# Optimization experiments

Measured on AMD Instinct MI355X. Metric: run time of the kernel, lower is better.

The kernel has to match this reference:

```python
import jax, jax.numpy as jnp
import numpy as np

B_GRAPHS, N2, FDIM, HEADS = 128, 32, 256, 4
TOTAL = 262144


def setup_inputs() -> dict:
    key = jax.random.key(0)
    ks = jax.random.split(key, 6)
    # sorted graph ids, guaranteed to cover all B_GRAPHS values
    batch = jnp.sort(jnp.concatenate([
        jax.random.randint(ks[0], (TOTAL - B_GRAPHS,), 0, B_GRAPHS),
        jnp.arange(B_GRAPHS)])).astype(jnp.int32)
    x = jax.random.normal(ks[1], (TOTAL, FDIM), jnp.float32)
    queries = jax.random.normal(ks[2], (1, N2, FDIM), jnp.float32)
    s = 1.0 / np.sqrt(FDIM)
    in_proj_w = jax.random.uniform(ks[3], (3 * FDIM, FDIM), jnp.float32, -s, s)
    in_proj_b = jnp.zeros((3 * FDIM,), jnp.float32)
    out_proj_w = jax.random.uniform(ks[4], (FDIM, FDIM), jnp.float32, -s, s)
    out_proj_b = jnp.zeros((FDIM,), jnp.float32)
    return {"x": x, "batch": batch, "queries": queries,
            "in_proj_w": in_proj_w, "in_proj_b": in_proj_b,
            "out_proj_w": out_proj_w, "out_proj_b": out_proj_b}


def reference(x, batch, queries, in_proj_w, in_proj_b, out_proj_w, out_proj_b):
    F = x.shape[-1]
    H = HEADS
    d = F // H
    B = int(batch.max()) + 1
    counts = jnp.bincount(batch, length=B)                      # [B]
    N_max = int(counts.max())
    offsets = jnp.concatenate([jnp.zeros((1,), counts.dtype), jnp.cumsum(counts)[:-1]])
    pos = jnp.arange(batch.shape[0]) - offsets[batch]           # position within segment
    # ragged -> padded scatter (equivalent of the python loop)
    x_padded = jnp.zeros((B, N_max, F), x.dtype).at[batch, pos].set(x)
    valid = jnp.arange(N_max)[None, :] < counts[:, None]        # [B, N_max], True = real token

    Wq, Wk, Wv = in_proj_w[:F], in_proj_w[F:2 * F], in_proj_w[2 * F:]
    bq, bk, bv = in_proj_b[:F], in_proj_b[F:2 * F], in_proj_b[2 * F:]

    scale = 1.0 / np.sqrt(d)
    q = (queries[0] @ Wq.T + bq).reshape(N2, H, d) * scale      # [N2, H, d] (shared over B)
    k = (x_padded @ Wk.T + bk).reshape(B, N_max, H, d)
    v = (x_padded @ Wv.T + bv).reshape(B, N_max, H, d)

    scores = jnp.einsum('qhd,bkhd->bhqk', q, k)                 # [B, H, N2, N_max]
    scores = jnp.where(valid[:, None, None, :], scores, -jnp.inf)
    attn = jax.nn.softmax(scores, axis=-1)
    out = jnp.einsum('bhqk,bkhd->bqhd', attn, v).reshape(B, N2, F)
    out = out @ out_proj_w.T + out_proj_b
    return out.reshape(B * N2, F)
```

## Files before the change

### kernel.cpp

```cpp
#include <hip/hip_runtime.h>
#include <hip/hip_bf16.h>

typedef __bf16 bf16x8 __attribute__((ext_vector_type(8)));
typedef float  f32x4  __attribute__((ext_vector_type(4)));

#define MFMA16(a,b,c) __builtin_amdgcn_mfma_f32_16x16x32_bf16((a),(b),(c),0,0,0)

__device__ __forceinline__ unsigned short f2bf(float f){
  unsigned int u = __float_as_uint(f);
  u += 0x7fffu + ((u >> 16) & 1u);
  return (unsigned short)(u >> 16);
}

__device__ __forceinline__ unsigned int cvtpk(float lo, float hi){
  unsigned int r;
  asm("v_cvt_pk_bf16_f32 %0, %1, %2" : "=v"(r) : "v"(lo), "v"(hi));
  return r;
}

__device__ __forceinline__ void block_sync(){
  asm volatile("s_waitcnt lgkmcnt(0)" ::: "memory");
  __builtin_amdgcn_s_barrier();
}

constexpr float SCALE_LOG2E = 0.125f * 1.4426950408889634f;

__global__ void k_prep(const float* __restrict__ queries, const float* __restrict__ ipw,
                       const float* __restrict__ ipb, const float* __restrict__ opw,
                       const float* __restrict__ opb, const int* __restrict__ batch,
                       int total, int* __restrict__ starts,
                       unsigned short* __restrict__ AqF,
                       unsigned short* __restrict__ Cmat, float* __restrict__ cvec)
{
  __shared__ __align__(16) float sh[256];
  __shared__ __align__(16) float sh2[256];
  const int t = threadIdx.x, bid = blockIdx.x;

  if (bid < 32){
    const int q = bid;
    sh[t] = queries[q*256 + t];
    __syncthreads();
    const float* wr = ipw + (size_t)t*256;
    float acc = 0.f;
    #pragma unroll 8
    for (int j = 0; j < 256; j += 4){
      float4 wv = *reinterpret_cast<const float4*>(wr + j);
      float4 qv = *reinterpret_cast<const float4*>(&sh[j]);
      acc += wv.x*qv.x + wv.y*qv.y + wv.z*qv.z + wv.w*qv.w;
    }
    sh2[t] = acc + ipb[t];
    __syncthreads();
    #pragma unroll
    for (int h = 0; h < 4; h++){
      const float* wk = ipw + (size_t)(256 + h*64)*256 + t;
      float a2 = 0.f;
      #pragma unroll 8
      for (int d = 0; d < 64; d++) a2 += sh2[h*64 + d] * wk[(size_t)d*256];
      const int dst = ((h*2 + (q>>4))*8 + (t>>5))*512 + (((t>>3)&3)*16 + (q&15))*8 + (t&7);
      AqF[dst] = f2bf(a2 * SCALE_LOG2E);
    }
  } else if (bid < 288){
    const int g = bid - 32;
    sh[t] = opw[(size_t)g*256 + t];
    __syncthreads();
    #pragma unroll
    for (int h = 0; h < 4; h++){
      const float* wv = ipw + (size_t)(512 + h*64)*256 + t;
      float acc = 0.f;
      #pragma unroll 8
      for (int d = 0; d < 64; d++) acc += wv[(size_t)d*256] * sh[h*64 + d];
      Cmat[(size_t)g*1024 + h*256 + t] = f2bf(acc);
    }
    sh2[t] = ipb[512 + t] * sh[t];
    __syncthreads();
    for (int off = 128; off > 0; off >>= 1){
      if (t < off) sh2[t] += sh2[t + off];
      __syncthreads();
    }
    if (t == 0) cvec[g] = sh2[0] + opb[g];
  } else {
    const int sb = bid - 288;
    const int i0 = sb*1024 + t*4;
    if (i0 + 3 < total){
      if (i0 == 0) starts[0] = 0;
      const int4 b4 = *reinterpret_cast<const int4*>(batch + i0);
      if (b4.y != b4.x) starts[b4.y] = i0 + 1;
      if (b4.z != b4.y) starts[b4.z] = i0 + 2;
      if (b4.w != b4.z) starts[b4.w] = i0 + 3;
      if (i0 + 4 < total){
        const int nxt = batch[i0 + 4];
        if (nxt != b4.w) starts[nxt] = i0 + 4;
      } else {
        starts[128] = total;
      }
    }
  }
}


#define LOADC(c_) { \
  const int c0_ = (c_)*32; \
  _Pragma("unroll") \
  for (int n = 0; n < 4; n++){ \
    int nl_ = c0_ + nq*4 + n; nl_ = nl_ < cnt-1 ? nl_ : cnt-1; \
    rA[n] = *reinterpret_cast<const float2*>(xg + (size_t)nl_*256 + fp*2); } }

#define STAGE(xsP, xtP) { \
  _Pragma("unroll") \
  for (int n = 0; n < 4; n++) \
    *reinterpret_cast<unsigned int*>(&(xsP)[(nq*4 + n)*264 + fp*2]) = cvtpk(rA[n].x, rA[n].y); \
  { const int f0_ = fp*2; \
    uint2 w0_; w0_.x = cvtpk(rA[0].x, rA[1].x); w0_.y = cvtpk(rA[2].x, rA[3].x); \
    *reinterpret_cast<uint2*>(reinterpret_cast<char*>(xtP) + ((f0_*80 + nq*8) ^ (((f0_>>2)&7)<<4))) = w0_; \
    const int f1_ = fp*2 + 1; \
    uint2 w1_; w1_.x = cvtpk(rA[0].y, rA[1].y); w1_.y = cvtpk(rA[2].y, rA[3].y); \
    *reinterpret_cast<uint2*>(reinterpret_cast<char*>(xtP) + ((f1_*80 + nq*8) ^ (((f1_>>2)&7)<<4))) = w1_; } }

__global__ __launch_bounds__(1024, 4) void k_attn(
    const float* __restrict__ x, const int* __restrict__ starts,
    const unsigned short* __restrict__ AqF,
    float* __restrict__ partO, float* __restrict__ partL)
{
  __shared__ __align__(16) unsigned short xsub[2][32*264];
  __shared__ __align__(16) unsigned short xT  [3][256*40];
  __shared__ __align__(16) unsigned short Plds[2][128*40];
  __shared__ __align__(16) float lred[2][128];

  const int tid = threadIdx.x;
  const int wave = tid >> 6, lane = tid & 63, lg = lane >> 4, li = lane & 15;
  const int nq = tid >> 7, fp = tid & 127;
  const int bid = blockIdx.x;
  const int g = bid >> 1, s = bid & 1;
  const int s0 = starts[g], s1 = starts[g+1];
  const int cntg = s1 - s0;
  const int half = (cntg + 1) >> 1;
  const int nstart = s0 + s*half;
  int cnt = cntg - s*half; cnt = cnt < 0 ? 0 : (cnt > half ? half : cnt);
  const int chunks = (cnt + 31) >> 5;
  const float* xg = x + (size_t)nstart*256;
  const int pbase = bid*128;

  float2 rA[4];
  if (chunks > 0){
    LOADC(0);
    STAGE(xsub[0], xT[0]);
    if (chunks > 1) LOADC(1);
    block_sync();
  }

  if (wave < 8){
    const int rg2 = wave >> 1, bsel = wave & 1;
    bf16x8 bfragS[2][8];
    #pragma unroll
    for (int rf = 0; rf < 2; rf++)
      #pragma unroll
      for (int kb = 0; kb < 8; kb++)
        bfragS[rf][kb] = *reinterpret_cast<const bf16x8*>(AqF + (size_t)((rg2*2 + rf)*8 + kb)*512 + lane*8);

    float rsum0 = 0.f, rsum1 = 0.f;
    const int row0 = rg2*32 + li, row1 = rg2*32 + 16 + li;
    const int pbyte0 = (row0*80 + bsel*32 + lg*8) ^ (((row0>>2)&7)<<4);
    const int pbyte1 = (row1*80 + bsel*32 + lg*8) ^ (((row1>>2)&7)<<4);

    int cur3 = 0;
    for (int c = 0; c < chunks; ++c){
      const int cur2 = c & 1;
      const int nxt3 = (cur3 == 2) ? 0 : cur3 + 1;

      f32x4 sc0 = f32x4{0.f,0.f,0.f,0.f}, sc1 = f32x4{0.f,0.f,0.f,0.f};
      __builtin_amdgcn_s_setprio(1);
      #pragma unroll
      for (int kb = 0; kb < 8; kb++){
        const bf16x8 af = *reinterpret_cast<const bf16x8*>(&xsub[cur2][(bsel*16 + li)*264 + kb*32 + lg*8]);
        sc0 = MFMA16(af, bfragS[0][kb], sc0);
        sc1 = MFMA16(af, bfragS[1][kb], sc1);
      }
      __builtin_amdgcn_s_setprio(0);

      const int nodebase = c*32 + bsel*16 + lg*4;
      float p0[4], p1[4];
      #pragma unroll
      for (int r = 0; r < 4; r++){
        const bool v = (nodebase + r) < cnt;
        p0[r] = v ? __builtin_exp2f(sc0[r]) : 0.f;
        p1[r] = v ? __builtin_exp2f(sc1[r]) : 0.f;
        rsum0 += p0[r]; rsum1 += p1[r];
      }
      {
        char* pl = reinterpret_cast<char*>(Plds[cur2]);
        uint2 w0; w0.x = cvtpk(p0[0], p0[1]); w0.y = cvtpk(p0[2], p0[3]);
        uint2 w1; w1.x = cvtpk(p1[0], p1[1]); w1.y = cvtpk(p1[2], p1[3]);
        *reinterpret_cast<uint2*>(pl + pbyte0) = w0;
        *reinterpret_cast<uint2*>(pl + pbyte1) = w1;
      }

      if (c + 1 < chunks){
        STAGE(xsub[cur2 ^ 1], xT[nxt3]);
        if (c + 2 < chunks) LOADC(c + 2);
      }
      block_sync();
      cur3 = nxt3;
    }

    rsum0 += __shfl_xor(rsum0, 16); rsum0 += __shfl_xor(rsum0, 32);
    rsum1 += __shfl_xor(rsum1, 16); rsum1 += __shfl_xor(rsum1, 32);
    if (lane < 16){
      lred[bsel][rg2*32 + li]      = rsum0;
      lred[bsel][rg2*32 + 16 + li] = rsum1;
    }
  } else {
    const int pw = wave - 8, fs = pw*32;
    f32x4 oacc[8][2];
    #pragma unroll
    for (int i = 0; i < 8; i++){ oacc[i][0] = f32x4{0.f,0.f,0.f,0.f}; oacc[i][1] = f32x4{0.f,0.f,0.f,0.f}; }
    const int fr0 = fs + li, fr1 = fs + 16 + li;
    const int bvb0 = (fr0*80 + lg*16) ^ (((fr0>>2)&7)<<4);
    const int bvb1 = (fr1*80 + lg*16) ^ (((fr1>>2)&7)<<4);

    int cur3 = 0;
    for (int c = 0; c < chunks; ++c){
      const int cur2 = c & 1;
      const int nxt3 = (cur3 == 2) ? 0 : cur3 + 1;

      if (c + 1 < chunks){
        STAGE(xsub[cur2 ^ 1], xT[nxt3]);
        if (c + 2 < chunks) LOADC(c + 2);
      }
      block_sync();

      const char* xtC = reinterpret_cast<const char*>(xT[cur3]);
      const bf16x8 bv0 = *reinterpret_cast<const bf16x8*>(xtC + bvb0);
      const bf16x8 bv1 = *reinterpret_cast<const bf16x8*>(xtC + bvb1);
      const char* plC = reinterpret_cast<const char*>(Plds[cur2]);
      __builtin_amdgcn_s_setprio(1);
      #pragma unroll
      for (int rt = 0; rt < 8; rt++){
        const int prow = rt*16 + li;
        const bf16x8 pa = *reinterpret_cast<const bf16x8*>(plC + ((prow*80 + lg*16) ^ (((prow>>2)&7)<<4)));
        oacc[rt][0] = MFMA16(pa, bv0, oacc[rt][0]);
        oacc[rt][1] = MFMA16(pa, bv1, oacc[rt][1]);
      }
      __builtin_amdgcn_s_setprio(0);
      cur3 = nxt3;
    }

    #pragma unroll
    for (int rt = 0; rt < 8; rt++){
      #pragma unroll
      for (int r = 0; r < 4; r++){
        const size_t orow = (size_t)(pbase + rt*16 + lg*4 + r)*256;
        partO[orow + fs + li]      = oacc[rt][0][r];
        partO[orow + fs + 16 + li] = oacc[rt][1][r];
      }
    }
  }

  block_sync();
  if (tid < 128) partL[pbase + tid] = lred[0][tid] + lred[1][tid];
}

__global__ __launch_bounds__(512, 1) void k_out(
    const float* __restrict__ partO, const float* __restrict__ partL,
    const unsigned short* __restrict__ Cmat, const float* __restrict__ cvec,
    float* __restrict__ out)
{
  __shared__ __align__(16) unsigned short plds[16*1024];
  __shared__ float sinv[64];
  const int tid = threadIdx.x;
  const int g = blockIdx.x >> 1, qh = blockIdx.x & 1;
  const int p0 = 2*g, p1 = 2*g + 1;
  if (tid < 64){
    const int h = tid >> 4, qr = tid & 15;
    const int row = h*32 + qh*16 + qr;
    const float L = partL[p0*128 + row] + partL[p1*128 + row];
    sinv[tid] = 1.f / L;
  }
  __syncthreads();
  #pragma unroll
  for (int i = 0; i < 8; i++){
    const int idx = tid + i*512;
    const int qr = idx >> 8;
    const int cg = idx & 255;
    const int h = cg >> 6, f4 = (cg & 63)*4;
    const int row = h*32 + qh*16 + qr;
    const float4 o0 = *reinterpret_cast<const float4*>(&partO[(size_t)(p0*128 + row)*256 + f4]);
    const float4 o1 = *reinterpret_cast<const float4*>(&partO[(size_t)(p1*128 + row)*256 + f4]);
    const float sc = sinv[h*16 + qr];
    uint2 w; w.x = cvtpk((o0.x+o1.x)*sc, (o0.y+o1.y)*sc);
             w.y = cvtpk((o0.z+o1.z)*sc, (o0.w+o1.w)*sc);
    const int col4 = cg*4;
    const int bc = (col4*2) ^ ((qr & 7) << 4);
    *reinterpret_cast<uint2*>(reinterpret_cast<char*>(plds) + qr*2048 + bc) = w;
  }
  __syncthreads();
  const int wave = tid >> 6, lane = tid & 63, lg = lane >> 4, li = lane & 15;
  f32x4 acc0 = {0.f,0.f,0.f,0.f}, acc1 = {0.f,0.f,0.f,0.f};
  const float cv0 = cvec[wave*32 + li], cv1 = cvec[wave*32 + 16 + li];
  const unsigned short* cb0 = Cmat + (size_t)(wave*32 + li)*1024;
  const unsigned short* cb1 = Cmat + (size_t)(wave*32 + 16 + li)*1024;
  #pragma unroll 8
  for (int kb = 0; kb < 32; kb++){
    const int bc = ((kb*32 + lg*8)*2) ^ ((li & 7) << 4);
    const bf16x8 aa = *reinterpret_cast<const bf16x8*>(reinterpret_cast<const char*>(plds) + li*2048 + bc);
    const bf16x8 b0 = *reinterpret_cast<const bf16x8*>(cb0 + kb*32 + lg*8);
    const bf16x8 b1 = *reinterpret_cast<const bf16x8*>(cb1 + kb*32 + lg*8);
    acc0 = MFMA16(aa, b0, acc0);
    acc1 = MFMA16(aa, b1, acc1);
  }
  #pragma unroll
  for (int r = 0; r < 4; r++){
    const int q = lg*4 + r;
    const size_t orow = (size_t)(g*32 + qh*16 + q)*256;
    out[orow + wave*32 + li]      = acc0[r] + cv0;
    out[orow + wave*32 + 16 + li] = acc1[r] + cv1;
  }
}


extern "C" void kernel_launch(void* const* d_in, const int* in_sizes, int n_in,
                              void* d_out, int out_size, void* d_ws, size_t ws_size,
                              hipStream_t stream)
{
  const float* x       = (const float*)d_in[0];
  const int*   batch   = (const int*)d_in[1];
  const float* queries = (const float*)d_in[2];
  const float* ipw     = (const float*)d_in[3];
  const float* ipb     = (const float*)d_in[4];
  const float* opw     = (const float*)d_in[5];
  const float* opb     = (const float*)d_in[6];
  float* out = (float*)d_out;
  const int total = in_sizes[1];

  char* w = (char*)d_ws;
  int*            starts = (int*)(w);
  unsigned short* AqF    = (unsigned short*)(w + 36*1024);
  unsigned short* Cmat   = (unsigned short*)(w + 102*1024);
  float*          cvec   = (float*)(w + 616*1024);
  float*          partO  = (float*)(w + (size_t)1024*1024);
  float*          partL  = (float*)(w + (size_t)1024*1024 + (size_t)256*128*256*4);

  k_prep<<<544, 256, 0, stream>>>(queries, ipw, ipb, opw, opb, batch, total,
                                  starts, AqF, Cmat, cvec);
  k_attn<<<256, 1024, 0, stream>>>(x, starts, AqF, partO, partL);
  k_out<<<256, 512, 0, stream>>>(partO, partL, Cmat, cvec, out);
}
```

Baseline: 105.0 us.

## Specialize producer waves for x staging and retile PV MFMA to 4x4

Moves all global loads and bf16 staging of x chunks from every wave to only the eight PV waves. Each of those waves now loads eight rows per chunk and keeps two register buffers, so prefetch runs two chunks ahead. The score waves no longer stage and only compute QK^T and exp. The PV waves switch from an 8x2 to a 4x4 MFMA tile over 64 rows by 64 features, so each loaded fragment is reused more. The cost is more register pressure and more load and convert work per PV wave, which may unbalance the two wave groups.

```diff
diff --git a/kernel.cpp b/kernel.cpp
--- a/kernel.cpp
+++ b/kernel.cpp
@@ -98,23 +98,28 @@
 }
 
 
-#define LOADC(c_) { \
+#define LOADC(dst, c_) { \
   const int c0_ = (c_)*32; \
   _Pragma("unroll") \
-  for (int n = 0; n < 4; n++){ \
-    int nl_ = c0_ + nq*4 + n; nl_ = nl_ < cnt-1 ? nl_ : cnt-1; \
-    rA[n] = *reinterpret_cast<const float2*>(xg + (size_t)nl_*256 + fp*2); } }
-
-#define STAGE(xsP, xtP) { \
+  for (int n = 0; n < 8; n++){ \
+    int nl_ = c0_ + nq*8 + n; nl_ = nl_ < cnt-1 ? nl_ : cnt-1; \
+    dst[n] = *reinterpret_cast<const float2*>(xg + (size_t)nl_*256 + fp*2); } }
+
+#define STAGE(xsP, xtP, src) { \
   _Pragma("unroll") \
-  for (int n = 0; n < 4; n++) \
-    *reinterpret_cast<unsigned int*>(&(xsP)[(nq*4 + n)*264 + fp*2]) = cvtpk(rA[n].x, rA[n].y); \
-  { const int f0_ = fp*2; \
-    uint2 w0_; w0_.x = cvtpk(rA[0].x, rA[1].x); w0_.y = cvtpk(rA[2].x, rA[3].x); \
-    *reinterpret_cast<uint2*>(reinterpret_cast<char*>(xtP) + ((f0_*80 + nq*8) ^ (((f0_>>2)&7)<<4))) = w0_; \
-    const int f1_ = fp*2 + 1; \
-    uint2 w1_; w1_.x = cvtpk(rA[0].y, rA[1].y); w1_.y = cvtpk(rA[2].y, rA[3].y); \
-    *reinterpret_cast<uint2*>(reinterpret_cast<char*>(xtP) + ((f1_*80 + nq*8) ^ (((f1_>>2)&7)<<4))) = w1_; } }
+  for (int n = 0; n < 8; n++) \
+    *reinterpret_cast<unsigned int*>(&(xsP)[(nq*8 + n)*264 + fp*2]) = cvtpk(src[n].x, src[n].y); \
+  { const int f0_ = fp*2; const int sw0 = ((f0_>>2)&7)<<4; const int b0 = f0_*80 + nq*16; \
+    uint2 wa, wb; \
+    wa.x = cvtpk(src[0].x, src[1].x); wa.y = cvtpk(src[2].x, src[3].x); \
+    wb.x = cvtpk(src[4].x, src[5].x); wb.y = cvtpk(src[6].x, src[7].x); \
+    *reinterpret_cast<uint2*>(reinterpret_cast<char*>(xtP) + ( b0      ^ sw0)) = wa; \
+    *reinterpret_cast<uint2*>(reinterpret_cast<char*>(xtP) + ((b0 + 8) ^ sw0)) = wb; \
+    const int f1_ = f0_ + 1; const int sw1 = ((f1_>>2)&7)<<4; const int b1 = f1_*80 + nq*16; \
+    wa.x = cvtpk(src[0].y, src[1].y); wa.y = cvtpk(src[2].y, src[3].y); \
+    wb.x = cvtpk(src[4].y, src[5].y); wb.y = cvtpk(src[6].y, src[7].y); \
+    *reinterpret_cast<uint2*>(reinterpret_cast<char*>(xtP) + ( b1      ^ sw1)) = wa; \
+    *reinterpret_cast<uint2*>(reinterpret_cast<char*>(xtP) + ((b1 + 8) ^ sw1)) = wb; } }
 
 __global__ __launch_bounds__(1024, 4) void k_attn(
     const float* __restrict__ x, const int* __restrict__ starts,
@@ -128,7 +133,7 @@
 
   const int tid = threadIdx.x;
   const int wave = tid >> 6, lane = tid & 63, lg = lane >> 4, li = lane & 15;
-  const int nq = tid >> 7, fp = tid & 127;
+  const int u = tid & 511, nq = u >> 7, fp = u & 127;
   const int bid = blockIdx.x;
   const int g = bid >> 1, s = bid & 1;
   const int s0 = starts[g], s1 = starts[g+1];
@@ -140,14 +145,6 @@
   const float* xg = x + (size_t)nstart*256;
   const int pbase = bid*128;
 
-  float2 rA[4];
-  if (chunks > 0){
-    LOADC(0);
-    STAGE(xsub[0], xT[0]);
-    if (chunks > 1) LOADC(1);
-    block_sync();
-  }
-
   if (wave < 8){
     const int rg2 = wave >> 1, bsel = wave & 1;
     bf16x8 bfragS[2][8];
@@ -162,10 +159,10 @@
     const int pbyte0 = (row0*80 + bsel*32 + lg*8) ^ (((row0>>2)&7)<<4);
     const int pbyte1 = (row1*80 + bsel*32 + lg*8) ^ (((row1>>2)&7)<<4);
 
-    int cur3 = 0;
+    block_sync();
+
     for (int c = 0; c < chunks; ++c){
       const int cur2 = c & 1;
-      const int nxt3 = (cur3 == 2) ? 0 : cur3 + 1;
 
       f32x4 sc0 = f32x4{0.f,0.f,0.f,0.f}, sc1 = f32x4{0.f,0.f,0.f,0.f};
       __builtin_amdgcn_s_setprio(1);
@@ -193,13 +190,7 @@
         *reinterpret_cast<uint2*>(pl + pbyte0) = w0;
         *reinterpret_cast<uint2*>(pl + pbyte1) = w1;
       }
-
-      if (c + 1 < chunks){
-        STAGE(xsub[cur2 ^ 1], xT[nxt3]);
-        if (c + 2 < chunks) LOADC(c + 2);
-      }
       block_sync();
-      cur3 = nxt3;
     }
 
     rsum0 += __shfl_xor(rsum0, 16); rsum0 += __shfl_xor(rsum0, 32);
@@ -209,48 +200,70 @@
       lred[bsel][rg2*32 + 16 + li] = rsum1;
     }
   } else {
-    const int pw = wave - 8, fs = pw*32;
-    f32x4 oacc[8][2];
-    #pragma unroll
-    for (int i = 0; i < 8; i++){ oacc[i][0] = f32x4{0.f,0.f,0.f,0.f}; oacc[i][1] = f32x4{0.f,0.f,0.f,0.f}; }
-    const int fr0 = fs + li, fr1 = fs + 16 + li;
-    const int bvb0 = (fr0*80 + lg*16) ^ (((fr0>>2)&7)<<4);
-    const int bvb1 = (fr1*80 + lg*16) ^ (((fr1>>2)&7)<<4);
-
-    int cur3 = 0;
+    const int pw = wave - 8;
+    const int rbase = (pw & 1) * 64;
+    const int fbase = (pw >> 1) * 64;
+    f32x4 oacc[4][4];
+    #pragma unroll
+    for (int i = 0; i < 4; i++)
+      #pragma unroll
+      for (int j = 0; j < 4; j++) oacc[i][j] = f32x4{0.f,0.f,0.f,0.f};
+
+    int bvb[4], pab[4];
+    #pragma unroll
+    for (int t4 = 0; t4 < 4; t4++){
+      const int fr = fbase + t4*16 + li;
+      bvb[t4] = (fr*80 + lg*16) ^ (((fr>>2)&7)<<4);
+      const int pr = rbase + t4*16 + li;
+      pab[t4] = (pr*80 + lg*16) ^ (((pr>>2)&7)<<4);
+    }
+
+    float2 rE[8], rO[8];
+    if (chunks > 0){
+      LOADC(rE, 0);
+      if (chunks > 1) LOADC(rO, 1);
+      STAGE(xsub[0], xT[0], rE);
+      if (chunks > 2) LOADC(rE, 2);
+    }
+    block_sync();
+
+    int wr3 = 1;
     for (int c = 0; c < chunks; ++c){
-      const int cur2 = c & 1;
-      const int nxt3 = (cur3 == 2) ? 0 : cur3 + 1;
-
+      const int cur3 = (wr3 == 0) ? 2 : wr3 - 1;
       if (c + 1 < chunks){
-        STAGE(xsub[cur2 ^ 1], xT[nxt3]);
-        if (c + 2 < chunks) LOADC(c + 2);
+        unsigned short* xsP = xsub[(c + 1) & 1];
+        unsigned short* xtP = xT[wr3];
+        if ((c + 1) & 1){ STAGE(xsP, xtP, rO); if (c + 3 < chunks) LOADC(rO, c + 3); }
+        else            { STAGE(xsP, xtP, rE); if (c + 3 < chunks) LOADC(rE, c + 3); }
       }
       block_sync();
 
       const char* xtC = reinterpret_cast<const char*>(xT[cur3]);
-      const bf16x8 bv0 = *reinterpret_cast<const bf16x8*>(xtC + bvb0);
-      const bf16x8 bv1 = *reinterpret_cast<const bf16x8*>(xtC + bvb1);
-      const char* plC = reinterpret_cast<const char*>(Plds[cur2]);
+      const char* plC = reinterpret_cast<const char*>(Plds[c & 1]);
+      bf16x8 bv[4];
+      #pragma unroll
+      for (int ft = 0; ft < 4; ft++)
+        bv[ft] = *reinterpret_cast<const bf16x8*>(xtC + bvb[ft]);
       __builtin_amdgcn_s_setprio(1);
       #pragma unroll
-      for (int rt = 0; rt < 8; rt++){
-        const int prow = rt*16 + li;
-        const bf16x8 pa = *reinterpret_cast<const bf16x8*>(plC + ((prow*80 + lg*16) ^ (((prow>>2)&7)<<4)));
-        oacc[rt][0] = MFMA16(pa, bv0, oacc[rt][0]);
-        oacc[rt][1] = MFMA16(pa, bv1, oacc[rt][1]);
+      for (int rt = 0; rt < 4; rt++){
+        const bf16x8 pa = *reinterpret_cast<const bf16x8*>(plC + pab[rt]);
+        #pragma unroll
+        for (int ft = 0; ft < 4; ft++)
+          oacc[rt][ft] = MFMA16(pa, bv[ft], oacc[rt][ft]);
       }
       __builtin_amdgcn_s_setprio(0);
-      cur3 = nxt3;
-    }
-
-    #pragma unroll
-    for (int rt = 0; rt < 8; rt++){
+      wr3 = (wr3 == 2) ? 0 : wr3 + 1;
+    }
+
+    #pragma unroll
+    for (int rt = 0; rt < 4; rt++){
       #pragma unroll
       for (int r = 0; r < 4; r++){
-        const size_t orow = (size_t)(pbase + rt*16 + lg*4 + r)*256;
-        partO[orow + fs + li]      = oacc[rt][0][r];
-        partO[orow + fs + 16 + li] = oacc[rt][1][r];
+        const size_t orow = (size_t)(pbase + rbase + rt*16 + lg*4 + r)*256;
+        #pragma unroll
+        for (int ft = 0; ft < 4; ft++)
+          partO[orow + fbase + ft*16 + li] = oacc[rt][ft][r];
       }
     }
   }
```

Measured after the change: 148.0 us. 40.9% more time.
